# Optimization experiments

Measured on AMD Instinct MI355X. Metric: run time of the kernel, lower is better.

The kernel has to match this reference:

```python
import jax, jax.numpy as jnp
import numpy as np

D_MODEL = 256
GAMMA = 0.9          # ret_D is built in the torch forward but never applied to the output; kept for fidelity notes
SCALE_BASE = 512     # XPOS default
TEMP = 10000.0
TWO_PI = 2.0 * np.pi


def sine_pos_embed(x):
    """DETR-style 1D sine position embedding with an all-ones mask (as in forward).
    x: [B,T,C] -> pos: [1,T,C] (mask is [1,T] ones, so batch dim broadcasts)."""
    T, C = x.shape[1], x.shape[2]
    x_embed = jnp.arange(1, T + 1, dtype=jnp.float32)          # cumsum of ones
    x_embed = x_embed / (x_embed[-1] + 1e-6) * TWO_PI          # normalize=True
    dim_t = TEMP ** (2.0 * (jnp.arange(C) // 2).astype(jnp.float32) / C)
    pos = x_embed[:, None] / dim_t                             # [T,C]
    pos = jnp.stack([jnp.sin(pos[:, 0::2]), jnp.cos(pos[:, 1::2])], axis=2).reshape(T, C)
    return pos[None].astype(x.dtype)


def _dup_interleave(m):
    # [L, d/2] -> [L, d], columns repeated pairwise: [a,b] -> [a,a,b,b]
    return jnp.repeat(m, 2, axis=-1)


def _rotate_every_two(x):
    x1, x2 = x[..., 0::2], x[..., 1::2]
    return jnp.stack([-x2, x1], axis=-1).reshape(x.shape)


def xpos_apply(x, downscale=False):
    """RetNet XPOS rotary embedding. x: [B,L,d]."""
    L, d = x.shape[1], x.shape[2]
    half = d // 2
    scale_vec = (jnp.arange(0, d, 2, dtype=jnp.float32) + 0.4 * d) / (1.4 * d)   # [d/2]
    power = jnp.arange(L, dtype=jnp.float32) / SCALE_BASE
    scale = scale_vec[None, :] ** power[:, None]                                  # [L, d/2]
    inv_freq = 1.0 / (TEMP ** (jnp.arange(half, dtype=jnp.float32) / half))
    sinusoid = jnp.arange(L, dtype=jnp.float32)[:, None] * inv_freq[None, :]      # [L, d/2]
    sin, cos = jnp.sin(sinusoid), jnp.cos(sinusoid)
    if downscale:
        scale = 1.0 / scale
    sin_s = _dup_interleave(sin * scale)[None].astype(x.dtype)   # [1,L,d]
    cos_s = _dup_interleave(cos * scale)[None].astype(x.dtype)
    return x * cos_s + _rotate_every_two(x) * sin_s


def setup_inputs() -> dict:
    key = jax.random.key(0)
    ks = jax.random.split(key, 8)
    B, TXT, VID, D = 16, 32, 2048, D_MODEL
    S = TXT + VID
    inp = {
        "src": jax.random.normal(ks[0], (B, S, D), dtype=jnp.float32),
        "learn_vid_ret": jax.random.normal(ks[1], (VID * VID, 1), dtype=jnp.float32),
        "W_txt_Q": jax.random.normal(ks[2], (D, D), dtype=jnp.float32) / D,
        "W_txt_K": jax.random.normal(ks[3], (D, D), dtype=jnp.float32) / D,
        "W_txt_V": jax.random.normal(ks[4], (D, D), dtype=jnp.float32) / D,
        "W_vid_Q": jax.random.normal(ks[5], (D, D), dtype=jnp.float32) / D,
        "W_vid_K": jax.random.normal(ks[6], (D, D), dtype=jnp.float32) / D,
        "W_vid_V": jax.random.normal(ks[7], (D, D), dtype=jnp.float32) / D,
        "txt_length": TXT,
    }
    return inp


def reference(src, learn_vid_ret, W_txt_Q, W_txt_K, W_txt_V, W_vid_Q, W_vid_K, W_vid_V, txt_length):
    S = src.shape[1]
    vid_length = S - txt_length

    # learned retention mask over the video block
    learn_ret = jax.nn.sigmoid(learn_vid_ret.reshape(vid_length, vid_length))
    diag = jnp.eye(vid_length, dtype=src.dtype)
    video_ret = (1.0 - diag) * learn_ret
    loss_sparsity = jnp.mean(jnp.abs(video_ret))

    # full [S,S] mask: ones everywhere, sigmoid(learned) on the vid-vid block
    ret_mask = jnp.ones((S, S), dtype=src.dtype).at[txt_length:, txt_length:].set(learn_ret)

    txt_mem = src[:, :txt_length]   # [B,TXT,D]
    vid_mem = src[:, txt_length:]   # [B,VID,D]

    pos = sine_pos_embed(txt_mem)   # [1,TXT,D]
    txt_Q = (pos + txt_mem) @ W_txt_Q
    txt_K = (pos + txt_mem) @ W_txt_K
    vid_Q = xpos_apply(vid_mem @ W_vid_Q)
    vid_K = xpos_apply(vid_mem @ W_vid_K, downscale=True)

    Q = jnp.concatenate([txt_Q, vid_Q], axis=1)                  # [B,S,D]
    K = jnp.concatenate([txt_K, vid_K], axis=1)                  # [B,S,D]
    V = jnp.concatenate([txt_mem @ W_txt_V, vid_mem @ W_vid_V], axis=1)

    # retention: QK^T elementwise-masked (no softmax), then weighted V sum
    scores = jnp.einsum('bsd,btd->bst', Q, K) * ret_mask[None]   # [B,S,S]
    out = scores @ V                                             # [B,S,D]
    return out, loss_sparsity
```

## Files before the change

kernel.cpp:

```cpp
#include <hip/hip_runtime.h>

#define B_   16
#define TXT  32
#define VID  2048
#define D_   256
#define S_   2080
#define SP   2176
#define NKT  34
#define GTOT 17424

typedef unsigned short ushort_t;
typedef __attribute__((ext_vector_type(8))) short short8;
typedef __attribute__((ext_vector_type(4))) short short4v;
typedef __attribute__((ext_vector_type(4))) float f32x4;
typedef __attribute__((ext_vector_type(16))) float f32x16;

__device__ __forceinline__ ushort_t f2bf(float f) {
  unsigned u = __builtin_bit_cast(unsigned, f);
  unsigned r = (u + 0x7FFFu + ((u >> 16) & 1u)) >> 16;
  return (ushort_t)r;
}
__device__ __forceinline__ float bf2f(ushort_t h) {
  unsigned u = ((unsigned)h) << 16;
  return __builtin_bit_cast(float, u);
}

__device__ __forceinline__ void g2l16(void* lds, const void* g) {
  __builtin_amdgcn_global_load_lds(
      (const __attribute__((address_space(1))) char*)g,
      (__attribute__((address_space(3))) char*)lds, 16, 0, 0);
}

__device__ __forceinline__ f32x4 mfma16(short8 a, short8 b, f32x4 c) {
  return __builtin_amdgcn_mfma_f32_16x16x32_bf16(a, b, c, 0, 0, 0);
}
__device__ __forceinline__ f32x16 mfma32(short8 a, short8 b, f32x16 c) {
  return __builtin_amdgcn_mfma_f32_32x32x16_bf16(a, b, c, 0, 0, 0);
}


__global__ void prep_kernel(const float* __restrict__ src, const float* __restrict__ learn,
                            const float* __restrict__ Wtq, const float* __restrict__ Wtk,
                            const float* __restrict__ Wtv,
                            const float* __restrict__ Wvq, const float* __restrict__ Wvk,
                            const float* __restrict__ Wvv,
                            ushort_t* __restrict__ Qs, ushort_t* __restrict__ Ks,
                            ushort_t* __restrict__ VTs, ushort_t* __restrict__ sigp,
                            float* __restrict__ tbl, ushort_t* __restrict__ WT,
                            float* __restrict__ loss) {
  __shared__ float shf[64 * 68];
  const int blk = blockIdx.x;
  const int tid = threadIdx.x;

  if (blk < 64) {
    float (*a_s)[256] = (float(*)[256])shf;
    float (*x_s)[256] = (float(*)[256])(shf + 2048);
    const int tg = blk & 3;
    const int b  = blk >> 2;
    const int c  = tid;
    #pragma unroll
    for (int t = 0; t < 8; ++t) {
      int row = tg * 8 + t;
      float x = src[((size_t)b * S_ + row) * D_ + c];
      float xe = (float)(row + 1) * (6.283185307179586f / (32.0f + 1e-6f));
      int i = c >> 1;
      float dimt = powf(10000.0f, (2.0f * (float)i) / 256.0f);
      float ang = xe / dimt;
      float pv = (c & 1) ? cosf(ang) : sinf(ang);
      x_s[t][c] = x;
      a_s[t][c] = x + pv;
    }
    __syncthreads();
    float q[8] = {0,0,0,0,0,0,0,0}, k[8] = {0,0,0,0,0,0,0,0}, v[8] = {0,0,0,0,0,0,0,0};
    for (int kk = 0; kk < 256; ++kk) {
      float wq = Wtq[(size_t)kk * 256 + c];
      float wk = Wtk[(size_t)kk * 256 + c];
      float wv = Wtv[(size_t)kk * 256 + c];
      #pragma unroll
      for (int t = 0; t < 8; ++t) {
        q[t] = fmaf(a_s[t][kk], wq, q[t]);
        k[t] = fmaf(a_s[t][kk], wk, k[t]);
        v[t] = fmaf(x_s[t][kk], wv, v[t]);
      }
    }
    #pragma unroll
    for (int t = 0; t < 8; ++t) {
      int row = tg * 8 + t;
      size_t base = ((size_t)(b * NKT)) << 14;
      size_t sub = (size_t)(c >> 4) * 1024 + row * 16 + (c & 15);
      Qs[base + sub] = f2bf(q[t]);
      Ks[base + sub] = f2bf(k[t]);
      VTs[base + (size_t)(row >> 4) * 4096 + c * 16 + (row & 15)] = f2bf(v[t]);
    }
  } else if (blk < 112) {
    float (*t)[68] = (float(*)[68])shf;
    const int m = blk - 64;
    const int k0 = (m & 3) * 64, n0 = ((m >> 2) & 3) * 64, mt = m >> 4;
    const float* W = (mt == 0) ? Wvq : (mt == 1) ? Wvk : Wvv;
    int r = tid >> 4, cq = (tid & 15) * 4;
    #pragma unroll
    for (int mm = 0; mm < 4; ++mm) {
      int k = mm * 16 + r;
      float4 v = *(const float4*)(W + (size_t)(k0 + k) * 256 + n0 + cq);
      t[k][cq] = v.x; t[k][cq + 1] = v.y; t[k][cq + 2] = v.z; t[k][cq + 3] = v.w;
    }
    __syncthreads();
    #pragma unroll
    for (int mm = 0; mm < 4; ++mm) {
      int n = mm * 16 + r;
      short4v h;
      h[0] = (short)f2bf(t[cq + 0][n]);
      h[1] = (short)f2bf(t[cq + 1][n]);
      h[2] = (short)f2bf(t[cq + 2][n]);
      h[3] = (short)f2bf(t[cq + 3][n]);
      *(short4v*)(WT + ((size_t)mt * D_ + n0 + n) * D_ + k0 + cq) = h;
    }
  } else if (blk < 1136) {
    int idx = (blk - 112) * 256 + tid;
    int n = idx >> 7, i = idx & 127;
    float invf = powf(10000.0f, -(float)i / 128.0f);
    float ang = (float)n * invf;
    float s, co;
    sincosf(ang, &s, &co);
    float sv = ((float)(2 * i) + 102.4f) / 358.4f;
    float sc = powf(sv, (float)n / 512.0f);
    float4 r;
    r.x = co * sc; r.y = s * sc; r.z = co / sc; r.w = s / sc;
    *(float4*)(tbl + (size_t)idx * 4) = r;
  } else if (blk < 1328) {
    int i = (blk - 1136) * 256 + tid;
    short8 z = {0, 0, 0, 0, 0, 0, 0, 0};
    int sec = i >> 14;
    int j = i & 16383;
    int bb = j >> 10;
    int rem = j & 1023;
    size_t base = ((size_t)(bb * NKT + 32)) << 14;
    if (sec == 0) {
      int kstep = rem >> 6, ch = rem & 63;
      *(short8*)(Qs + base + kstep * 1024 + 512 + ch * 8) = z;
    } else if (sec == 1) {
      int kstep = rem >> 6, ch = rem & 63;
      *(short8*)(Ks + base + kstep * 1024 + 512 + ch * 8) = z;
    } else {
      *(short8*)(VTs + base + 8192 + rem * 8) = z;
    }
  } else {
    float* red = shf;
    const int base = ((blk - 1328) * 256 + tid) * 8;
    float4 v0 = *(const float4*)(learn + base);
    float4 v1 = *(const float4*)(learn + base + 4);
    float vals[8] = {v0.x, v0.y, v0.z, v0.w, v1.x, v1.y, v1.z, v1.w};
    float acc = 0.f;
    short8 sh;
    #pragma unroll
    for (int j = 0; j < 8; ++j) {
      int idx = base + j;
      float s = 1.0f / (1.0f + expf(-vals[j]));
      sh[j] = (short)f2bf(s);
      int rr = idx >> 11, cc = idx & 2047;
      if (rr != cc) acc += s;
    }
    *(short8*)(sigp + base) = sh;
    red[tid] = acc;
    __syncthreads();
    #pragma unroll
    for (int st = 128; st > 0; st >>= 1) {
      if (tid < st) red[tid] += red[tid + st];
      __syncthreads();
    }
    if (tid == 0) atomicAdd(loss, red[0] * (1.0f / 4194304.0f));
  }
}

__global__ void cvt_kernel(const float* __restrict__ src, ushort_t* __restrict__ srcb) {
  int i = blockIdx.x * 256 + threadIdx.x;
  int b = i >> 16;
  int rem = i & 65535;
  int row = rem >> 5, c8 = (rem & 31) * 8;
  const float* p = src + ((size_t)b * S_ + TXT + row) * D_ + c8;
  float4 v0 = *(const float4*)p;
  float4 v1 = *(const float4*)(p + 4);
  short8 h;
  h[0] = (short)f2bf(v0.x); h[1] = (short)f2bf(v0.y); h[2] = (short)f2bf(v0.z); h[3] = (short)f2bf(v0.w);
  h[4] = (short)f2bf(v1.x); h[5] = (short)f2bf(v1.y); h[6] = (short)f2bf(v1.z); h[7] = (short)f2bf(v1.w);
  *(short8*)(srcb + ((size_t)b * VID + row) * D_ + c8) = h;
}

template <int MODE>
__global__ __launch_bounds__(256, 2) void vid_gemm(
    const float* __restrict__ src, const ushort_t* __restrict__ srcb,
    const ushort_t* __restrict__ WT, const float* __restrict__ tbl,
    ushort_t* __restrict__ Qs, ushort_t* __restrict__ Ks, ushort_t* __restrict__ VTs) {
  __shared__ __align__(16) ushort_t ldsA[64 * 64];
  __shared__ __align__(16) ushort_t ldsB[64 * 64];

  const int rt = blockIdx.x;
  const int b  = blockIdx.y;
  const int ct = blockIdx.z;
  const int nt = ct >> 2;
  const int n0 = (ct & 3) * 64;
  const int tid = threadIdx.x;
  const int wv = tid >> 6, lane = tid & 63, l15 = lane & 15, l4 = lane >> 4;

  f32x4 acc[4];
  #pragma unroll
  for (int t2 = 0; t2 < 4; ++t2) { acc[t2][0] = 0.f; acc[t2][1] = 0.f; acc[t2][2] = 0.f; acc[t2][3] = 0.f; }

  for (int kk = 0; kk < 256; kk += 64) {
    if (MODE == 1) {
      #pragma unroll
      for (int m = 0; m < 2; ++m) {
        int p = (m * 256 + tid) * 16;
        int r = p >> 7;
        int cb = (p & 127) ^ ((r & 7) << 4);
        g2l16((char*)ldsA + p,
              (const char*)(srcb + ((size_t)b * VID + rt * 64 + r) * D_ + kk) + cb);
      }
    } else {
      #pragma unroll
      for (int m = 0; m < 4; ++m) {
        int q = m * 256 + tid;
        int r = q >> 4;
        int kc = (q & 15) * 4;
        const float4 v = *(const float4*)(src + ((size_t)b * S_ + TXT + rt * 64 + r) * D_ + kk + kc);
        short4v h;
        h[0] = (short)f2bf(v.x); h[1] = (short)f2bf(v.y);
        h[2] = (short)f2bf(v.z); h[3] = (short)f2bf(v.w);
        int off = ((r << 7) + (kc << 1)) ^ ((r & 7) << 4);
        *(short4v*)((char*)ldsA + off) = h;
      }
    }
    #pragma unroll
    for (int m = 0; m < 2; ++m) {
      int p = (m * 256 + tid) * 16;
      int nl = p >> 7;
      int c = (p & 127) ^ ((nl & 7) << 4);
      g2l16((char*)ldsB + p, (const char*)(WT + ((size_t)nt * D_ + n0 + nl) * D_ + kk) + c);
    }
    __syncthreads();
    #pragma unroll
    for (int ks = 0; ks < 2; ++ks) {
      int ar = wv * 16 + l15;
      int aoff = ((ar << 7) + ((ks * 32 + l4 * 8) << 1)) ^ ((ar & 7) << 4);
      short8 av = *(const short8*)((const char*)ldsA + aoff);
      #pragma unroll
      for (int t2 = 0; t2 < 4; ++t2) {
        int nl = t2 * 16 + l15;
        int boff = ((nl << 7) + ((ks * 32 + l4 * 8) << 1)) ^ ((nl & 7) << 4);
        short8 bv = *(const short8*)((const char*)ldsB + boff);
        acc[t2] = mfma16(av, bv, acc[t2]);
      }
    }
    __syncthreads();
  }

  const int rowl = wv * 16 + l4 * 4;
  if (nt < 2) {
    #pragma unroll
    for (int t2 = 0; t2 < 4; ++t2) {
      int c = n0 + t2 * 16 + l15;
      #pragma unroll
      for (int r = 0; r < 4; ++r) {
        int n = rt * 64 + rowl + r;
        float x = acc[t2][r];
        float xp = __shfl_xor(x, 1);
        const float4 tb = *(const float4*)(tbl + ((size_t)n * 128 + (c >> 1)) * 4);
        float cs = (nt == 0) ? tb.x : tb.z;
        float ss = (nt == 0) ? tb.y : tb.w;
        float val = (c & 1) ? fmaf(x, cs, xp * ss) : fmaf(x, cs, -xp * ss);
        int rowg = TXT + n;
        size_t idx = (((size_t)(b * NKT + (rowg >> 6))) << 14)
                   + (size_t)(c >> 4) * 1024 + (rowg & 63) * 16 + (c & 15);
        if (nt == 0) Qs[idx] = f2bf(val);
        else         Ks[idx] = f2bf(val);
      }
    }
  } else {
    #pragma unroll
    for (int t2 = 0; t2 < 4; ++t2)
      #pragma unroll
      for (int r = 0; r < 4; ++r) {
        int rr = rowl + r;
        int cc = t2 * 16 + l15;
        int off = ((rr << 7) + (cc << 1)) ^ ((rr & 7) << 4);
        *(ushort_t*)((char*)ldsA + off) = f2bf(acc[t2][r]);
      }
    __syncthreads();
    int n = tid >> 2;
    int rc = (tid & 3) * 16;
    short8 o0, o1;
    #pragma unroll
    for (int j = 0; j < 8; ++j) {
      int rr = rc + j;
      int off = ((rr << 7) + (n << 1)) ^ ((rr & 7) << 4);
      o0[j] = *(const short*)((const char*)ldsA + off);
    }
    #pragma unroll
    for (int j = 0; j < 8; ++j) {
      int rr = rc + 8 + j;
      int off = ((rr << 7) + (n << 1)) ^ ((rr & 7) << 4);
      o1[j] = *(const short*)((const char*)ldsA + off);
    }
    int d = n0 + n;
    int kvg0 = TXT + rt * 64 + rc;
    size_t base = (((size_t)(b * NKT + (kvg0 >> 6))) << 14) + ((kvg0 >> 4) & 3) * 4096 + d * 16;
    *(short8*)(VTs + base) = o0;
    *(short8*)(VTs + base + 8) = o1;
  }
}

__global__ __launch_bounds__(256, 2) void attn_kernel(
    const ushort_t* __restrict__ Qs, const ushort_t* __restrict__ Ks,
    const ushort_t* __restrict__ VTs, const ushort_t* __restrict__ sigp,
    float* __restrict__ out) {
  __shared__ __align__(16) ushort_t Kb[16384];
  __shared__ __align__(16) ushort_t Vb[16384];
  __shared__ __align__(16) ushort_t Pb[4096];

  const int kblk = blockIdx.x;
  const int bs = (kblk & 7) * 64 + (kblk >> 3);
  int g = bs * 34 + (bs >> 5);
  const int gend = (bs + 1) * 34 + ((bs + 1) >> 5);

  const int tid = threadIdx.x;
  const int wid = tid >> 6, lane = tid & 63;
  const int l31 = lane & 31, l5 = lane >> 5;
  const int qh = wid >> 1, kh = wid & 1;
  const int d0 = wid * 64;
  const int qloc = qh * 32 + l31;
  const int pkey = (l31 & 15) << 4;

  int b = g / 1089, rem = g - b * 1089, qt = rem / 33, kvt = rem - qt * 33;

  short8 qf[16];
  int4 mq[4];

  auto ldq = [&](int bb, int qq) {
    const ushort_t* qb = Qs + (((size_t)(bb * NKT + qq)) << 14) + qloc * 16 + l5 * 8;
    #pragma unroll
    for (int ks = 0; ks < 16; ++ks) qf[ks] = *(const short8*)(qb + ks * 1024);
  };
  auto ldmask = [&](int qq, int tt) {
    int q = qq * 64 + qloc;
    int qc = q - TXT; qc = qc < 0 ? 0 : (qc > 2047 ? 2047 : qc);
    int kvp = tt * 64 + kh * 32 - TXT;
    int kvc = (kvp >= 0 && kvp <= 2016) ? kvp : 0;
    const int4* mrow = (const int4*)(sigp + (size_t)qc * 2048 + kvc);
    mq[0] = mrow[0]; mq[1] = mrow[1]; mq[2] = mrow[2]; mq[3] = mrow[3];
  };
  auto stageK = [&](int bb, int tt) {
    const char* src = (const char*)Ks + (((size_t)(bb * NKT + tt)) << 15);
    #pragma unroll
    for (int m = 0; m < 8; ++m) { int s2 = m * 256 + tid; g2l16((char*)Kb + s2 * 16, src + s2 * 16); }
  };
  auto stageV = [&](int bb, int tt) {
    const char* src = (const char*)VTs + (((size_t)(bb * NKT + tt)) << 15);
    #pragma unroll
    for (int m = 0; m < 8; ++m) { int s2 = m * 256 + tid; g2l16((char*)Vb + s2 * 16, src + s2 * 16); }
  };

  f32x16 oacc[2][2];
  #pragma unroll
  for (int i2 = 0; i2 < 2; ++i2)
    #pragma unroll
    for (int j2 = 0; j2 < 2; ++j2)
      #pragma unroll
      for (int r = 0; r < 16; ++r) oacc[i2][j2][r] = 0.f;

  auto flushO = [&](int bb, int qq) {
    #pragma unroll
    for (int qg2 = 0; qg2 < 2; ++qg2)
      #pragma unroll
      for (int dg = 0; dg < 2; ++dg)
        #pragma unroll
        for (int r = 0; r < 16; ++r) {
          int qg = qq * 64 + qg2 * 32 + (r & 3) + 8 * (r >> 2) + 4 * l5;
          int dd = d0 + dg * 32 + l31;
          if (qg < S_)
            unsafeAtomicAdd(&out[((size_t)bb * S_ + qg) * D_ + dd], oacc[qg2][dg][r]);
          oacc[qg2][dg][r] = 0.f;
        }
  };

  stageK(b, kvt);
  ldmask(qt, kvt);
  stageV(b, kvt);
  ldq(b, qt);
  asm volatile("s_waitcnt vmcnt(0)" ::: "memory");
  __builtin_amdgcn_sched_barrier(0);
  __builtin_amdgcn_s_barrier();
  __builtin_amdgcn_sched_barrier(0);

  while (g < gend) {
    int gn = (g + 1 < GTOT) ? g + 1 : GTOT - 1;
    int nb = gn / 1089, nrem = gn - nb * 1089, nqt = nrem / 33, nkvt = nrem - nqt * 33;

    f32x16 s0, s1;
    #pragma unroll
    for (int r = 0; r < 16; ++r) { s0[r] = 0.f; s1[r] = 0.f; }
    const int arow = (kh * 32 + l31) * 32 + l5 * 16;
    __builtin_amdgcn_s_setprio(1);
    #pragma unroll
    for (int ks = 0; ks < 8; ++ks) {
      short8 ka = *(const short8*)((const char*)Kb + ks * 2048 + arow);
      short8 kc = *(const short8*)((const char*)Kb + (ks + 8) * 2048 + arow);
      s0 = mfma32(ka, qf[ks], s0);
      s1 = mfma32(kc, qf[ks + 8], s1);
    }
    __builtin_amdgcn_s_setprio(0);

    {
      int q = qt * 64 + qloc;
      bool qv = (q >= TXT) && (q < S_);
      int kvp = kvt * 64 + kh * 32 - TXT;
      bool kvv = (kvp >= 0 && kvp <= 2016);
      bool ok = qv && kvv;
      const unsigned* mw = (const unsigned*)mq;
      #pragma unroll
      for (int t = 0; t < 4; ++t) {
        unsigned w0p, w1p;
        {
          unsigned wa = mw[4 * t + 0], wb = mw[4 * t + 2];
          unsigned w = l5 ? wb : wa;
          float m0 = ok ? bf2f((ushort_t)(w & 0xFFFFu)) : 1.0f;
          float m1 = ok ? bf2f((ushort_t)(w >> 16)) : 1.0f;
          int r = 4 * t;
          float p0 = (s0[r] + s1[r]) * m0;
          float p1 = (s0[r + 1] + s1[r + 1]) * m1;
          asm("v_cvt_pk_bf16_f32 %0, %1, %2" : "=v"(w0p) : "v"(p0), "v"(p1));
        }
        {
          unsigned wa = mw[4 * t + 1], wb = mw[4 * t + 3];
          unsigned w = l5 ? wb : wa;
          float m0 = ok ? bf2f((ushort_t)(w & 0xFFFFu)) : 1.0f;
          float m1 = ok ? bf2f((ushort_t)(w >> 16)) : 1.0f;
          int r = 4 * t + 2;
          float p0 = (s0[r] + s1[r]) * m0;
          float p1 = (s0[r + 1] + s1[r + 1]) * m1;
          asm("v_cvt_pk_bf16_f32 %0, %1, %2" : "=v"(w1p) : "v"(p0), "v"(p1));
        }
        int off = (l31 << 8) + (((qh << 7) + (kh << 6) + (t << 4) + (l5 << 3)) ^ pkey);
        *(uint2*)((char*)Pb + off) = make_uint2(w0p, w1p);
      }
    }

    asm volatile("s_waitcnt vmcnt(0) lgkmcnt(0)" ::: "memory");
    __builtin_amdgcn_sched_barrier(0);
    __builtin_amdgcn_s_barrier();
    __builtin_amdgcn_sched_barrier(0);

    stageK(nb, nkvt);
    __builtin_amdgcn_sched_barrier(0);

    __builtin_amdgcn_s_setprio(1);
    #pragma unroll
    for (int ks = 0; ks < 4; ++ks) {
      int p0 = (l31 << 8) + ((ks * 32 + l5 * 16) ^ pkey);
      int p1 = (l31 << 8) + ((128 + ks * 32 + l5 * 16) ^ pkey);
      short8 pf0 = *(const short8*)((const char*)Pb + p0);
      short8 pf1 = *(const short8*)((const char*)Pb + p1);
      short8 vf0 = *(const short8*)((const char*)Vb + ks * 8192 + (d0 + l31) * 32 + l5 * 16);
      short8 vf1 = *(const short8*)((const char*)Vb + ks * 8192 + (d0 + 32 + l31) * 32 + l5 * 16);
      oacc[0][0] = mfma32(pf0, vf0, oacc[0][0]);
      oacc[0][1] = mfma32(pf0, vf1, oacc[0][1]);
      oacc[1][0] = mfma32(pf1, vf0, oacc[1][0]);
      oacc[1][1] = mfma32(pf1, vf1, oacc[1][1]);
    }
    __builtin_amdgcn_s_setprio(0);
    asm volatile("s_waitcnt lgkmcnt(0)" ::: "memory");
    __builtin_amdgcn_sched_barrier(0);
    __builtin_amdgcn_s_barrier();
    __builtin_amdgcn_sched_barrier(0);

    ldmask(nqt, nkvt);
    __builtin_amdgcn_sched_barrier(0);
    const bool qchange = (nqt != qt || nb != b);
    if (qchange) {
      flushO(b, qt);
      ldq(nb, nqt);
    }
    __builtin_amdgcn_sched_barrier(0);
    stageV(nb, nkvt);
    __builtin_amdgcn_sched_barrier(0);
    if (qchange) { asm volatile("s_waitcnt vmcnt(24)" ::: "memory"); }
    else         { asm volatile("s_waitcnt vmcnt(12)" ::: "memory"); }
    __builtin_amdgcn_sched_barrier(0);
    __builtin_amdgcn_s_barrier();
    __builtin_amdgcn_sched_barrier(0);

    b = nb; qt = nqt; kvt = nkvt; ++g;
  }

  flushO(b, qt);
}

extern "C" void kernel_launch(void* const* d_in, const int* in_sizes, int n_in,
                              void* d_out, int out_size, void* d_ws, size_t ws_size,
                              hipStream_t stream) {
  (void)in_sizes; (void)n_in;
  const float* src   = (const float*)d_in[0];
  const float* learn = (const float*)d_in[1];
  const float* Wtq = (const float*)d_in[2];
  const float* Wtk = (const float*)d_in[3];
  const float* Wtv = (const float*)d_in[4];
  const float* Wvq = (const float*)d_in[5];
  const float* Wvk = (const float*)d_in[6];
  const float* Wvv = (const float*)d_in[7];
  float* out = (float*)d_out;

  char* ws = (char*)d_ws;
  const size_t QKV_ONE  = (size_t)B_ * SP * D_ * 2;
  const size_t QP_OFF   = 0;
  const size_t KS_OFF   = QP_OFF + QKV_ONE;
  const size_t VT_OFF   = KS_OFF + QKV_ONE;
  const size_t SIG_OFF  = VT_OFF + QKV_ONE;
  const size_t TBL_OFF  = SIG_OFF + (size_t)VID * VID * 2;
  const size_t WT_OFF   = TBL_OFF + (size_t)VID * 128 * 4 * sizeof(float);
  const size_t SRCB_OFF = WT_OFF + (size_t)3 * D_ * D_ * 2;
  const size_t NEED_SRCB = SRCB_OFF + (size_t)B_ * VID * D_ * 2;

  ushort_t* Qs   = (ushort_t*)(ws + QP_OFF);
  ushort_t* Ks   = (ushort_t*)(ws + KS_OFF);
  ushort_t* VTs  = (ushort_t*)(ws + VT_OFF);
  ushort_t* sigp = (ushort_t*)(ws + SIG_OFF);
  float*    tbl  = (float*)(ws + TBL_OFF);
  ushort_t* WT   = (ushort_t*)(ws + WT_OFF);
  ushort_t* srcb = (ushort_t*)(ws + SRCB_OFF);
  float*    loss = out + (size_t)B_ * S_ * D_;

  hipMemsetAsync(d_out, 0, (size_t)out_size * sizeof(float), stream);
  prep_kernel<<<3376, 256, 0, stream>>>(src, learn, Wtq, Wtk, Wtv, Wvq, Wvk, Wvv,
                                        Qs, Ks, VTs, sigp, tbl, WT, loss);
  if (ws_size >= NEED_SRCB) {
    cvt_kernel<<<4096, 256, 0, stream>>>(src, srcb);
    vid_gemm<1><<<dim3(32, B_, 12), 256, 0, stream>>>(src, srcb, WT, tbl, Qs, Ks, VTs);
  } else {
    vid_gemm<0><<<dim3(32, B_, 12), 256, 0, stream>>>(src, srcb, WT, tbl, Qs, Ks, VTs);
  }
  attn_kernel<<<dim3(512), 256, 0, stream>>>(Qs, Ks, VTs, sigp, out);
}
```

Baseline: 289.7 us.

## Load V fragments directly from global, drop V LDS buffer, raise occupancy

Removes the shared-memory V tile and its async staging. Each wave now loads its V MFMA fragments straight from global memory inside the PV loop. The mask load is narrowed to only the bytes each half-wave needs. With LDS use lower, launch bounds go from 2 to 4 blocks per CU, one barrier per iteration is dropped, and the vmcnt waits are adjusted. The trade is global-load latency inside the PV MFMA loop, which could stall it, and higher register pressure under the tighter launch bounds.

```diff
diff --git a/kernel.cpp b/kernel.cpp
--- a/kernel.cpp
+++ b/kernel.cpp
@@ -309,12 +309,11 @@
   }
 }
 
-__global__ __launch_bounds__(256, 2) void attn_kernel(
+__global__ __launch_bounds__(256, 4) void attn_kernel(
     const ushort_t* __restrict__ Qs, const ushort_t* __restrict__ Ks,
     const ushort_t* __restrict__ VTs, const ushort_t* __restrict__ sigp,
     float* __restrict__ out) {
   __shared__ __align__(16) ushort_t Kb[16384];
-  __shared__ __align__(16) ushort_t Vb[16384];
   __shared__ __align__(16) ushort_t Pb[4096];
 
   const int kblk = blockIdx.x;
@@ -333,7 +332,7 @@
   int b = g / 1089, rem = g - b * 1089, qt = rem / 33, kvt = rem - qt * 33;
 
   short8 qf[16];
-  int4 mq[4];
+  int2 mq[4];
 
   auto ldq = [&](int bb, int qq) {
     const ushort_t* qb = Qs + (((size_t)(bb * NKT + qq)) << 14) + qloc * 16 + l5 * 8;
@@ -345,18 +344,14 @@
     int qc = q - TXT; qc = qc < 0 ? 0 : (qc > 2047 ? 2047 : qc);
     int kvp = tt * 64 + kh * 32 - TXT;
     int kvc = (kvp >= 0 && kvp <= 2016) ? kvp : 0;
-    const int4* mrow = (const int4*)(sigp + (size_t)qc * 2048 + kvc);
-    mq[0] = mrow[0]; mq[1] = mrow[1]; mq[2] = mrow[2]; mq[3] = mrow[3];
+    const char* mrow = (const char*)(sigp + (size_t)qc * 2048 + kvc) + l5 * 8;
+    #pragma unroll
+    for (int t = 0; t < 4; ++t) mq[t] = *(const int2*)(mrow + 16 * t);
   };
   auto stageK = [&](int bb, int tt) {
     const char* src = (const char*)Ks + (((size_t)(bb * NKT + tt)) << 15);
     #pragma unroll
     for (int m = 0; m < 8; ++m) { int s2 = m * 256 + tid; g2l16((char*)Kb + s2 * 16, src + s2 * 16); }
-  };
-  auto stageV = [&](int bb, int tt) {
-    const char* src = (const char*)VTs + (((size_t)(bb * NKT + tt)) << 15);
-    #pragma unroll
-    for (int m = 0; m < 8; ++m) { int s2 = m * 256 + tid; g2l16((char*)Vb + s2 * 16, src + s2 * 16); }
   };
 
   f32x16 oacc[2][2];
@@ -384,7 +379,6 @@
 
   stageK(b, kvt);
   ldmask(qt, kvt);
-  stageV(b, kvt);
   ldq(b, qt);
   asm volatile("s_waitcnt vmcnt(0)" ::: "memory");
   __builtin_amdgcn_sched_barrier(0);
@@ -415,13 +409,11 @@
       int kvp = kvt * 64 + kh * 32 - TXT;
       bool kvv = (kvp >= 0 && kvp <= 2016);
       bool ok = qv && kvv;
-      const unsigned* mw = (const unsigned*)mq;
       #pragma unroll
       for (int t = 0; t < 4; ++t) {
         unsigned w0p, w1p;
         {
-          unsigned wa = mw[4 * t + 0], wb = mw[4 * t + 2];
-          unsigned w = l5 ? wb : wa;
+          unsigned w = (unsigned)mq[t].x;
           float m0 = ok ? bf2f((ushort_t)(w & 0xFFFFu)) : 1.0f;
           float m1 = ok ? bf2f((ushort_t)(w >> 16)) : 1.0f;
           int r = 4 * t;
@@ -430,8 +422,7 @@
           asm("v_cvt_pk_bf16_f32 %0, %1, %2" : "=v"(w0p) : "v"(p0), "v"(p1));
         }
         {
-          unsigned wa = mw[4 * t + 1], wb = mw[4 * t + 3];
-          unsigned w = l5 ? wb : wa;
+          unsigned w = (unsigned)mq[t].y;
           float m0 = ok ? bf2f((ushort_t)(w & 0xFFFFu)) : 1.0f;
           float m1 = ok ? bf2f((ushort_t)(w >> 16)) : 1.0f;
           int r = 4 * t + 2;
@@ -444,7 +435,7 @@
       }
     }
 
-    asm volatile("s_waitcnt vmcnt(0) lgkmcnt(0)" ::: "memory");
+    asm volatile("s_waitcnt lgkmcnt(0)" ::: "memory");
     __builtin_amdgcn_sched_barrier(0);
     __builtin_amdgcn_s_barrier();
     __builtin_amdgcn_sched_barrier(0);
@@ -452,15 +443,16 @@
     stageK(nb, nkvt);
     __builtin_amdgcn_sched_barrier(0);
 
+    const ushort_t* vb = VTs + (((size_t)(b * NKT + kvt)) << 14) + (size_t)d0 * 16 + l5 * 8;
     __builtin_amdgcn_s_setprio(1);
     #pragma unroll
     for (int ks = 0; ks < 4; ++ks) {
+      short8 vf0 = *(const short8*)(vb + ks * 4096 + l31 * 16);
+      short8 vf1 = *(const short8*)(vb + ks * 4096 + (l31 + 32) * 16);
       int p0 = (l31 << 8) + ((ks * 32 + l5 * 16) ^ pkey);
       int p1 = (l31 << 8) + ((128 + ks * 32 + l5 * 16) ^ pkey);
       short8 pf0 = *(const short8*)((const char*)Pb + p0);
       short8 pf1 = *(const short8*)((const char*)Pb + p1);
-      short8 vf0 = *(const short8*)((const char*)Vb + ks * 8192 + (d0 + l31) * 32 + l5 * 16);
-      short8 vf1 = *(const short8*)((const char*)Vb + ks * 8192 + (d0 + 32 + l31) * 32 + l5 * 16);
       oacc[0][0] = mfma32(pf0, vf0, oacc[0][0]);
       oacc[0][1] = mfma32(pf0, vf1, oacc[0][1]);
       oacc[1][0] = mfma32(pf1, vf0, oacc[1][0]);
@@ -469,21 +461,16 @@
     __builtin_amdgcn_s_setprio(0);
     asm volatile("s_waitcnt lgkmcnt(0)" ::: "memory");
     __builtin_amdgcn_sched_barrier(0);
-    __builtin_amdgcn_s_barrier();
-    __builtin_amdgcn_sched_barrier(0);
 
     ldmask(nqt, nkvt);
+    __builtin_amdgcn_sched_barrier(0);
+    asm volatile("s_waitcnt vmcnt(4)" ::: "memory");
     __builtin_amdgcn_sched_barrier(0);
     const bool qchange = (nqt != qt || nb != b);
     if (qchange) {
       flushO(b, qt);
       ldq(nb, nqt);
     }
-    __builtin_amdgcn_sched_barrier(0);
-    stageV(nb, nkvt);
-    __builtin_amdgcn_sched_barrier(0);
-    if (qchange) { asm volatile("s_waitcnt vmcnt(24)" ::: "memory"); }
-    else         { asm volatile("s_waitcnt vmcnt(12)" ::: "memory"); }
     __builtin_amdgcn_sched_barrier(0);
     __builtin_amdgcn_s_barrier();
     __builtin_amdgcn_sched_barrier(0);
```

New measurement: 650.4 us. 125% more time.
